# Kernel optimization log

Hardware: AMD Instinct MI355X
Metric: run time of the kernel (lower is better)

Reference implementation:

```python
import jax, jax.numpy as jnp
import numpy as np

STRIDE = (1, 1)
PADDING = (1, 1)
DILATION = (1, 1)


def deform_conv(x, offset, weight, stride=STRIDE, padding=PADDING, dilation=DILATION):
    """Deformable convolution v1 (mmcv layout), deformable_groups=1, groups=1.

    x:      [B, C, H, W]
    offset: [B, 2*kh*kw, Ho, Wo]   pairs ordered (dy, dx) per kernel tap
    weight: [Co, C, kh, kw]
    """
    B, C, H, W = x.shape
    Co, Ci, kh, kw = weight.shape
    sh, sw = stride
    ph, pw = padding
    dh, dw = dilation
    Ho = (H + 2 * ph - (dh * (kh - 1) + 1)) // sh + 1
    Wo = (W + 2 * pw - (dw * (kw - 1) + 1)) // sw + 1
    K2 = kh * kw

    off = offset.reshape(B, K2, 2, Ho, Wo)
    # base sampling grid per kernel tap: [K2, Ho, Wo]
    ky = (jnp.arange(K2) // kw) * dh          # kernel row offsets
    kx = (jnp.arange(K2) % kw) * dw           # kernel col offsets
    hi = jnp.arange(Ho) * sh - ph             # output-row -> input-row base
    wi = jnp.arange(Wo) * sw - pw
    py = off[:, :, 0] + (ky[:, None, None] + hi[None, :, None])  # [B,K2,Ho,Wo]
    px = off[:, :, 1] + (kx[:, None, None] + wi[None, None, :])  # [B,K2,Ho,Wo]

    y0 = jnp.floor(py)
    x0 = jnp.floor(px)
    ly = py - y0
    lx = px - x0
    hy = 1.0 - ly
    hx = 1.0 - lx
    y0i = y0.astype(jnp.int32)
    x0i = x0.astype(jnp.int32)
    y1i = y0i + 1
    x1i = x0i + 1

    xf = x.reshape(B, C, H * W)

    def gather(yi, xi):
        # zero padding outside the image, per-corner validity (DCN semantics)
        valid = (yi >= 0) & (yi < H) & (xi >= 0) & (xi < W)
        yc = jnp.clip(yi, 0, H - 1)
        xc = jnp.clip(xi, 0, W - 1)
        idx = (yc * W + xc).reshape(B, -1)                 # [B, K2*Ho*Wo]
        vals = jax.vmap(lambda xb, ib: xb[:, ib])(xf, idx)  # [B, C, K2*Ho*Wo]
        vals = vals.reshape(B, C, K2, Ho, Wo)
        return vals * valid[:, None].astype(x.dtype)

    # im2col with bilinear sampling: [B, C, K2, Ho, Wo]
    col = (gather(y0i, x0i) * (hy * hx)[:, None]
           + gather(y0i, x1i) * (hy * lx)[:, None]
           + gather(y1i, x0i) * (ly * hx)[:, None]
           + gather(y1i, x1i) * (ly * lx)[:, None])

    # GEMM: out[b,o,h,w] = sum_{c,k} W[o,c,k] * col[b,c,k,h,w]
    out = jnp.einsum('bckhw,ock->bohw', col, weight.reshape(Co, Ci, K2))
    return out


def setup_inputs() -> dict:
    key = jax.random.key(0)
    k1, k2, k3 = jax.random.split(key, 3)
    x = jax.random.normal(k1, (4, 256, 64, 64), dtype=jnp.float32)
    offset = jax.random.normal(k2, (4, 18, 64, 64), dtype=jnp.float32)
    n = 256 * 3 * 3
    stdv = 1.0 / np.sqrt(n)
    weight = jax.random.uniform(k3, (256, 256, 3, 3), dtype=jnp.float32,
                                minval=-stdv, maxval=stdv)
    return {"x": x, "offset": offset, "weight": weight}


def reference(x, offset, weight):
    return deform_conv(x, offset, weight)
```

## Files before the change

### kernel.cpp

```cpp
#include <hip/hip_runtime.h>
#include <hip/hip_bf16.h>
#include <cstddef>

#define B_    4
#define C_    256
#define H_    64
#define W_    64
#define CO_   256
#define K2_   9
#define NSTEP 72

typedef __attribute__((ext_vector_type(8))) short short8;
typedef __attribute__((ext_vector_type(4))) float f32x4;

__device__ __forceinline__ unsigned short f2bf(float f) {
    unsigned u = __builtin_bit_cast(unsigned, f);
    u = (u + 0x7fffu + ((u >> 16) & 1u)) >> 16;
    return (unsigned short)u;
}
__device__ __forceinline__ unsigned pack2bf(float lo, float hi) {
    __hip_bfloat162 h = __float22bfloat162_rn(make_float2(lo, hi));
    unsigned r; __builtin_memcpy(&r, &h, 4);
    return r;
}
__device__ __forceinline__ float bflo(unsigned u) {
    return __builtin_bit_cast(float, u << 16);
}
__device__ __forceinline__ float bfhi(unsigned u) {
    return __builtin_bit_cast(float, u & 0xffff0000u);
}

#if defined(__has_builtin)
#if __has_builtin(__builtin_amdgcn_fdot2_f32_bf16)
#define HAS_BFDOT2 1
#endif
#endif
__device__ __forceinline__ float dot2bf(unsigned x, unsigned w, float acc) {
#ifdef HAS_BFDOT2
    typedef __attribute__((ext_vector_type(2))) __bf16 bf16x2;
    return __builtin_amdgcn_fdot2_f32_bf16(__builtin_bit_cast(bf16x2, x),
                                           __builtin_bit_cast(bf16x2, w),
                                           acc, false);
#else
    return acc + bflo(x) * bflo(w) + bfhi(x) * bfhi(w);
#endif
}

__global__ void wpack_kernel(const float* __restrict__ w,
                             unsigned short* __restrict__ wpk) {
    const int idx = blockIdx.x * 256 + threadIdx.x;
    if (idx >= NSTEP * 16 * 64) return;
    const int lane = idx & 63;
    const int mt   = (idx >> 6) & 15;
    const int s    = idx >> 10;
    const int o    = mt * 16 + (lane & 15);
    const int cc   = s / 9;
    const int t    = s - 9 * cc;
    const int c0   = cc * 32 + ((lane >> 4) << 3);
    unsigned short h[8];
#pragma unroll
    for (int e = 0; e < 8; ++e)
        h[e] = f2bf(w[(o * C_ + c0 + e) * K2_ + t]);
    uint4 v;
    v.x = h[0] | ((unsigned)h[1] << 16);
    v.y = h[2] | ((unsigned)h[3] << 16);
    v.z = h[4] | ((unsigned)h[5] << 16);
    v.w = h[6] | ((unsigned)h[7] << 16);
    *reinterpret_cast<uint4*>(&wpk[(size_t)idx * 8]) = v;
}

__device__ __forceinline__ short8 loadA(const unsigned short* __restrict__ wpk,
                                        const float* __restrict__ wraw,
                                        int use_pk, int s, int mt, int lane) {
    if (use_pk) {
        return *reinterpret_cast<const short8*>(
            wpk + (((size_t)(s * 16 + mt) * 64 + lane) << 3));
    } else {
        const int cc = s / 9;
        const int t  = s - 9 * cc;
        const int c0 = cc * 32 + ((lane >> 4) << 3);
        const int o  = mt * 16 + (lane & 15);
        short8 r;
#pragma unroll
        for (int e = 0; e < 8; ++e)
            r[e] = (short)f2bf(wraw[(o * C_ + c0 + e) * K2_ + t]);
        return r;
    }
}

__global__ __launch_bounds__(512, 4)
void dcn_mfma_kernel(const float* __restrict__ x,
                     const float* __restrict__ off,
                     const unsigned short* __restrict__ wpk,
                     const float* __restrict__ wraw,
                     float* __restrict__ out,
                     int use_pk) {
    __shared__ __align__(16) unsigned s_win[32 * 484 + 48];
    __shared__ __align__(8)  unsigned s_mwp[K2_ * 32 * 2];
    __shared__ int s_menc[K2_ * 32];
    __shared__ __align__(16) unsigned short s_colb[2][1024];

    const int tid = threadIdx.x;
    const int bid = blockIdx.x;
    const int xcd  = bid & 7;
    const int slot = bid >> 3;
    const int b    = xcd >> 1;
    const int ho   = ((xcd & 1) << 5) | (slot >> 1);
    const int woh  = slot & 1;
    const int wo0  = woh << 5;

    const char* xb8 = (const char*)x + ((size_t)b << 22);

    if (tid < 48) s_win[32 * 484 + tid] = 0u;

    if (tid < K2_ * 32) {
        const int t = tid >> 5;
        const int p = tid & 31;
        const int pa = wo0 + p;
        const float dy = off[((b * 18 + 2 * t    ) * 64 + ho) * 64 + pa];
        const float dx = off[((b * 18 + 2 * t + 1) * 64 + ho) * 64 + pa];
        const float py = (float)(ho - 1 + t / 3) + dy;
        const float px = (float)(pa - 1 + t % 3) + dx;
        const float y0f = floorf(py), x0f = floorf(px);
        const float ly = py - y0f, lx = px - x0f;
        const float hy = 1.0f - ly, hx = 1.0f - lx;
        const int y0 = (int)y0f, x0 = (int)x0f;
        const int y1 = y0 + 1,   x1 = x0 + 1;
        const bool vy0 = (y0 >= 0) & (y0 < H_);
        const bool vy1 = (y1 >= 0) & (y1 < H_);
        const bool vx0 = (x0 >= 0) & (x0 < W_);
        const bool vx1 = (x1 >= 0) & (x1 < W_);
        const int yc0 = min(max(y0, 0), H_ - 1);
        const int yc1 = min(max(y1, 0), H_ - 1);
        const int xc0 = min(max(x0, 0), W_ - 1);
        const int xc1 = min(max(x1, 0), W_ - 1);
        float w00 = (vy0 && vx0) ? hy * hx : 0.0f;
        float w01 = (vy0 && vx1) ? hy * lx : 0.0f;
        float w10 = (vy1 && vx0) ? ly * hx : 0.0f;
        float w11 = (vy1 && vx1) ? ly * lx : 0.0f;
        const int dys = yc1 - yc0, dxs = xc1 - xc0;
        if (!dxs) { w00 += w01; w01 = 0.0f; w10 += w11; w11 = 0.0f; }
        if (!dys) { w00 += w10; w10 = 0.0f; w01 += w11; w11 = 0.0f; }
        const int r0 = yc0 - (ho - 5);
        const int j0 = xc0 - (wo0 - 8);
        const bool fast = (r0 >= 0) & (r0 + dys <= 10) & (j0 >= 0) & (j0 <= 43);
        int enc;
        if (fast)
            enc = (r0 * 44 + j0) << 2;
        else
            enc = (int)(0x80000000u
                        | (unsigned)((((yc0 << 6) + xc0) << 2) | (dys << 1) | dxs));
        s_mwp[(t * 32 + p) * 2    ] = pack2bf(w00, w01);
        s_mwp[(t * 32 + p) * 2 + 1] = pack2bf(w10, w11);
        s_menc[t * 32 + p] = enc;
    }

    unsigned stoff[8];
#pragma unroll
    for (int v = 0; v < 8; ++v) {
        const int u = tid + (v << 9);
        if (u < 3872) {
            const int cl  = u / 121;
            const int rem = u - cl * 121;
            const int r   = rem / 11;
            const int q   = rem - r * 11;
            const int y   = ho - 5 + r;
            int gof = (((y << 6) + wo0 - 8) << 2) + (q << 4);
            gof = min(max(gof, 0), 16368);
            if ((unsigned)y >= 64u) gof = 0;
            stoff[v] = ((unsigned)cl << 14) + (unsigned)gof;
        } else {
            stoff[v] = 0xffffffffu;
        }
    }

    const int lane = tid & 63;
    const int wave = tid >> 6;
    const int wo   = lane & 31;
    const int kk0  = (wave << 2) | ((lane >> 5) << 1);
    const unsigned swr = ((unsigned)(wo >> 4) << 10)
                       | ((unsigned)((wo & 15) | ((kk0 >> 3) << 4)) << 4)
                       | ((unsigned)(kk0 & 7) << 1);
    const unsigned brd = (unsigned)lane << 4;
    const int mt0 = wave << 1;
    const char* winC = (const char*)s_win + kk0 * 1936;
    const char* winD = winC + 1936;

    f32x4 acc[2][2];
#pragma unroll
    for (int m = 0; m < 2; ++m)
#pragma unroll
        for (int nt = 0; nt < 2; ++nt)
            acc[m][nt] = (f32x4)(0.0f);

#define STAGEW(XCB_) do {                                                      \
        char* wb_ = (char*)s_win + (size_t)tid * 16;                           \
        _Pragma("unroll")                                                      \
        for (int v_ = 0; v_ < 8; ++v_) {                                       \
            const unsigned so_ = stoff[v_];                                    \
            if (so_ != 0xffffffffu) {                                          \
                const float4 g_ = *(const float4*)((XCB_) + so_);              \
                const unsigned in_ = so_ & 16383u;                             \
                const float g4_ = *(const float*)((XCB_)                       \
                                    + (in_ >= 16368u ? so_ : so_ + 16));       \
                uint4 pk_;                                                     \
                pk_.x = pack2bf(g_.x, g_.y);                                   \
                pk_.y = pack2bf(g_.y, g_.z);                                   \
                pk_.z = pack2bf(g_.z, g_.w);                                   \
                pk_.w = pack2bf(g_.w, g4_);                                    \
                *(uint4*)(wb_ + v_ * 8192) = pk_;                              \
            }                                                                  \
        }                                                                      \
    } while (0)

#define COLT1(T_, BUFB_, XCB_) do {                                            \
        const unsigned u01_ = s_mwp[((T_) * 32 + wo) * 2];                     \
        const unsigned u23_ = s_mwp[((T_) * 32 + wo) * 2 + 1];                 \
        const int mb_ = s_menc[(T_) * 32 + wo];                                \
        float vA_, vB_;                                                        \
        if (__builtin_expect(mb_ >= 0, 1)) {                                   \
            const char* pA_ = winC + mb_;                                      \
            const char* pB_ = winD + mb_;                                      \
            const unsigned a0_ = *(const unsigned*)(pA_);                      \
            const unsigned a1_ = *(const unsigned*)(pA_ + 176);                \
            const unsigned c0_ = *(const unsigned*)(pB_);                      \
            const unsigned c1_ = *(const unsigned*)(pB_ + 176);                \
            vA_ = dot2bf(a1_, u23_, dot2bf(a0_, u01_, 0.0f));                  \
            vB_ = dot2bf(c1_, u23_, dot2bf(c0_, u01_, 0.0f));                  \
        } else {                                                               \
            const float w0_ = bflo(u01_), w1_ = bfhi(u01_);                    \
            const float w2_ = bflo(u23_), w3_ = bfhi(u23_);                    \
            const int dxb_ = (mb_ & 1) << 2, dyb_ = (mb_ & 2) << 7;            \
            const int o_ = mb_ & 0x3fffc;                                      \
            const char* plA_ = (XCB_) + ((size_t)kk0 << 14);                   \
            const char* plB_ = plA_ + (1 << 14);                               \
            vA_ = w0_ * *(const float*)(plA_ + o_)                             \
                + w1_ * *(const float*)(plA_ + o_ + dxb_)                      \
                + w2_ * *(const float*)(plA_ + o_ + dyb_)                      \
                + w3_ * *(const float*)(plA_ + o_ + dyb_ + dxb_);              \
            vB_ = w0_ * *(const float*)(plB_ + o_)                             \
                + w1_ * *(const float*)(plB_ + o_ + dxb_)                      \
                + w2_ * *(const float*)(plB_ + o_ + dyb_)                      \
                + w3_ * *(const float*)(plB_ + o_ + dyb_ + dxb_);              \
        }                                                                      \
        *(unsigned*)((char*)(BUFB_) + swr) = pack2bf(vA_, vB_);                \
    } while (0)

#define MFMA_(A_, B_, C_) __builtin_amdgcn_mfma_f32_16x16x32_bf16(A_, B_, C_, 0, 0, 0)

#define GEMM22(BUFB_) do {                                                     \
        const char* cb_ = (const char*)(BUFB_);                                \
        const short8 b0_ = *(const short8*)(cb_ + brd);                        \
        const short8 b1_ = *(const short8*)(cb_ + brd + 1024);                 \
        acc[0][0] = MFMA_(aC0, b0_, acc[0][0]);                                \
        acc[0][1] = MFMA_(aC0, b1_, acc[0][1]);                                \
        acc[1][0] = MFMA_(aC1, b0_, acc[1][0]);                                \
        acc[1][1] = MFMA_(aC1, b1_, acc[1][1]);                                \
    } while (0)

#define BARLG() do {                                                           \
        asm volatile("s_waitcnt lgkmcnt(0)" ::: "memory");                     \
        __builtin_amdgcn_s_barrier();                                          \
    } while (0)

    char* const buf0 = (char*)s_colb;
    char* const buf1 = (char*)s_colb + 2048;

    STAGEW(xb8);
    __syncthreads();
    COLT1(0, buf0, xb8);
    short8 aC0 = loadA(wpk, wraw, use_pk, 0, mt0,     lane);
    short8 aC1 = loadA(wpk, wraw, use_pk, 0, mt0 + 1, lane);
    BARLG();

    for (int cc = 0; cc < 8; ++cc) {
        const char* xcb  = xb8 + ((size_t)cc << 19);
        const char* xcbN = xb8 + ((size_t)(cc + 1) << 19);

#pragma unroll
        for (int j = 0; j < 9; ++j) {
            const int sj = cc * 9 + j;
            short8 aN0, aN1;
            const bool pf = (sj + 1 < NSTEP);
            if (pf) {
                aN0 = loadA(wpk, wraw, use_pk, sj + 1, mt0,     lane);
                aN1 = loadA(wpk, wraw, use_pk, sj + 1, mt0 + 1, lane);
            }
            if (j < 8) COLT1(j + 1, (j & 1) ? buf0 : buf1, xcb);
            GEMM22((j & 1) ? buf1 : buf0);
            BARLG();
            if (pf) { aC0 = aN0; aC1 = aN1; }
        }

        if (cc < 7) {
            STAGEW(xcbN);
            __syncthreads();
            COLT1(0, buf0, xcbN);
            BARLG();
        }
    }

#undef STAGEW
#undef COLT1
#undef MFMA_
#undef GEMM22
#undef BARLG

#pragma unroll
    for (int m = 0; m < 2; ++m) {
        const int ob = (mt0 + m) * 16 + ((lane >> 4) << 2);
#pragma unroll
        for (int r = 0; r < 4; ++r) {
            float* orow = out + (((size_t)(b * CO_ + ob + r) * 64 + ho) * 64 + wo0);
#pragma unroll
            for (int nt = 0; nt < 2; ++nt)
                orow[(nt << 4) | (lane & 15)] = acc[m][nt][r];
        }
    }
}

extern "C" void kernel_launch(void* const* d_in, const int* in_sizes, int n_in,
                              void* d_out, int out_size, void* d_ws, size_t ws_size,
                              hipStream_t stream) {
    const float* x      = (const float*)d_in[0];
    const float* offset = (const float*)d_in[1];
    const float* weight = (const float*)d_in[2];
    float* out = (float*)d_out;

    const size_t pk_bytes = (size_t)NSTEP * 16 * 64 * 8 * 2;
    const int use_pk = (ws_size >= pk_bytes) ? 1 : 0;
    unsigned short* wpk = (unsigned short*)d_ws;

    if (use_pk) {
        wpack_kernel<<<288, 256, 0, stream>>>(weight, wpk);
    }
    dcn_mfma_kernel<<<512, 512, 0, stream>>>(x, offset, wpk, weight, out, use_pk);
}
```

Measured before the change: 67.22 us.

## Process three kernel taps per barrier phase and overlap window staging with GEMM

Changes the per-tap double-buffered pipeline into phases of three taps, using triple-slot col buffers in each of two banks. This cuts the barrier count per channel chunk from about 9 to 4. The next chunk's window staging (STAGEW) now runs alongside the last phase's MFMAs instead of in a separate serialized step, which also removes one __syncthreads. In exchange the LDS col buffer grows threefold and more A-fragment registers are live at once, which could lower occupancy under launch_bounds(512,4).

```diff
diff --git a/kernel.cpp b/kernel.cpp
--- a/kernel.cpp
+++ b/kernel.cpp
@@ -98,7 +98,7 @@
     __shared__ __align__(16) unsigned s_win[32 * 484 + 48];
     __shared__ __align__(8)  unsigned s_mwp[K2_ * 32 * 2];
     __shared__ int s_menc[K2_ * 32];
-    __shared__ __align__(16) unsigned short s_colb[2][1024];
+    __shared__ __align__(16) unsigned short s_colb[2][3][1024];
 
     const int tid = threadIdx.x;
     const int bid = blockIdx.x;
@@ -213,7 +213,7 @@
         }                                                                      \
     } while (0)
 
-#define COLT1(T_, BUFB_, XCB_) do {                                            \
+#define COLT1(T_, DST_, XCB_) do {                                             \
         const unsigned u01_ = s_mwp[((T_) * 32 + wo) * 2];                     \
         const unsigned u23_ = s_mwp[((T_) * 32 + wo) * 2 + 1];                 \
         const int mb_ = s_menc[(T_) * 32 + wo];                                \
@@ -243,19 +243,19 @@
                 + w2_ * *(const float*)(plB_ + o_ + dyb_)                      \
                 + w3_ * *(const float*)(plB_ + o_ + dyb_ + dxb_);              \
         }                                                                      \
-        *(unsigned*)((char*)(BUFB_) + swr) = pack2bf(vA_, vB_);                \
+        *(unsigned*)((char*)(DST_) + swr) = pack2bf(vA_, vB_);                 \
     } while (0)
 
 #define MFMA_(A_, B_, C_) __builtin_amdgcn_mfma_f32_16x16x32_bf16(A_, B_, C_, 0, 0, 0)
 
-#define GEMM22(BUFB_) do {                                                     \
-        const char* cb_ = (const char*)(BUFB_);                                \
+#define GEMM22(SLOT_, A0_, A1_) do {                                           \
+        const char* cb_ = (const char*)(SLOT_);                                \
         const short8 b0_ = *(const short8*)(cb_ + brd);                        \
         const short8 b1_ = *(const short8*)(cb_ + brd + 1024);                 \
-        acc[0][0] = MFMA_(aC0, b0_, acc[0][0]);                                \
-        acc[0][1] = MFMA_(aC0, b1_, acc[0][1]);                                \
-        acc[1][0] = MFMA_(aC1, b0_, acc[1][0]);                                \
-        acc[1][1] = MFMA_(aC1, b1_, acc[1][1]);                                \
+        acc[0][0] = MFMA_(A0_, b0_, acc[0][0]);                                \
+        acc[0][1] = MFMA_(A0_, b1_, acc[0][1]);                                \
+        acc[1][0] = MFMA_(A1_, b0_, acc[1][0]);                                \
+        acc[1][1] = MFMA_(A1_, b1_, acc[1][1]);                                \
     } while (0)
 
 #define BARLG() do {                                                           \
@@ -263,39 +263,58 @@
         __builtin_amdgcn_s_barrier();                                          \
     } while (0)
 
-    char* const buf0 = (char*)s_colb;
-    char* const buf1 = (char*)s_colb + 2048;
+#define PHASE3(TC_, CDST_, TG_, GSRC_, XCB_) do {                              \
+        const short8 a00_ = loadA(wpk, wraw, use_pk, s0 + (TG_),     mt0,     lane); \
+        const short8 a01_ = loadA(wpk, wraw, use_pk, s0 + (TG_),     mt0 + 1, lane); \
+        const short8 a10_ = loadA(wpk, wraw, use_pk, s0 + (TG_) + 1, mt0,     lane); \
+        const short8 a11_ = loadA(wpk, wraw, use_pk, s0 + (TG_) + 1, mt0 + 1, lane); \
+        const short8 a20_ = loadA(wpk, wraw, use_pk, s0 + (TG_) + 2, mt0,     lane); \
+        const short8 a21_ = loadA(wpk, wraw, use_pk, s0 + (TG_) + 2, mt0 + 1, lane); \
+        COLT1((TC_),     (char*)(CDST_),        XCB_);                         \
+        COLT1((TC_) + 1, (char*)(CDST_) + 2048, XCB_);                         \
+        COLT1((TC_) + 2, (char*)(CDST_) + 4096, XCB_);                         \
+        GEMM22((char*)(GSRC_),        a00_, a01_);                             \
+        GEMM22((char*)(GSRC_) + 2048, a10_, a11_);                             \
+        GEMM22((char*)(GSRC_) + 4096, a20_, a21_);                             \
+        BARLG();                                                               \
+    } while (0)
 
     STAGEW(xb8);
     __syncthreads();
-    COLT1(0, buf0, xb8);
-    short8 aC0 = loadA(wpk, wraw, use_pk, 0, mt0,     lane);
-    short8 aC1 = loadA(wpk, wraw, use_pk, 0, mt0 + 1, lane);
+    COLT1(0, (char*)s_colb,        xb8);
+    COLT1(1, (char*)s_colb + 2048, xb8);
+    COLT1(2, (char*)s_colb + 4096, xb8);
     BARLG();
 
     for (int cc = 0; cc < 8; ++cc) {
         const char* xcb  = xb8 + ((size_t)cc << 19);
         const char* xcbN = xb8 + ((size_t)(cc + 1) << 19);
-
-#pragma unroll
-        for (int j = 0; j < 9; ++j) {
-            const int sj = cc * 9 + j;
-            short8 aN0, aN1;
-            const bool pf = (sj + 1 < NSTEP);
-            if (pf) {
-                aN0 = loadA(wpk, wraw, use_pk, sj + 1, mt0,     lane);
-                aN1 = loadA(wpk, wraw, use_pk, sj + 1, mt0 + 1, lane);
-            }
-            if (j < 8) COLT1(j + 1, (j & 1) ? buf0 : buf1, xcb);
-            GEMM22((j & 1) ? buf1 : buf0);
+        char* bufP = (char*)s_colb + (cc & 1) * 6144;
+        char* bufQ = (char*)s_colb + ((cc & 1) ^ 1) * 6144;
+        const int s0 = cc * 9;
+
+        PHASE3(3, bufQ, 0, bufP, xcb);
+
+        PHASE3(6, bufP, 3, bufQ, xcb);
+
+        {
+            const short8 a00_ = loadA(wpk, wraw, use_pk, s0 + 6, mt0,     lane);
+            const short8 a01_ = loadA(wpk, wraw, use_pk, s0 + 6, mt0 + 1, lane);
+            const short8 a10_ = loadA(wpk, wraw, use_pk, s0 + 7, mt0,     lane);
+            const short8 a11_ = loadA(wpk, wraw, use_pk, s0 + 7, mt0 + 1, lane);
+            const short8 a20_ = loadA(wpk, wraw, use_pk, s0 + 8, mt0,     lane);
+            const short8 a21_ = loadA(wpk, wraw, use_pk, s0 + 8, mt0 + 1, lane);
+            if (cc < 7) STAGEW(xcbN);
+            GEMM22(bufP,        a00_, a01_);
+            GEMM22(bufP + 2048, a10_, a11_);
+            GEMM22(bufP + 4096, a20_, a21_);
             BARLG();
-            if (pf) { aC0 = aN0; aC1 = aN1; }
         }
 
         if (cc < 7) {
-            STAGEW(xcbN);
-            __syncthreads();
-            COLT1(0, buf0, xcbN);
+            COLT1(0, bufQ,        xcbN);
+            COLT1(1, bufQ + 2048, xcbN);
+            COLT1(2, bufQ + 4096, xcbN);
             BARLG();
         }
     }
@@ -305,6 +324,7 @@
 #undef MFMA_
 #undef GEMM22
 #undef BARLG
+#undef PHASE3
 
 #pragma unroll
     for (int m = 0; m < 2; ++m) {
```

New measurement: 65.74 us. 1.02x faster.

## Batch all nine column taps per channel chunk and shrink staging window

Applied to the files above, without the earlier changes.

Each channel chunk now has all nine bilinear column tiles computed into nine LDS buffers at once. The GEMM then runs nine MFMA steps back-to-back with one barrier, replacing nine barriers per chunk. The next chunk's input window is staged into LDS while the GEMM reads the column buffers. The window drops from 11 to 10 rows, trimming LDS footprint and staging loads; more taps' samples may now take the slow global path. Weight-fragment prefetch is removed and fragments are loaded inline in the GEMM loop, which may expose load latency.

```diff
diff --git a/kernel.cpp b/kernel.cpp
--- a/kernel.cpp
+++ b/kernel.cpp
@@ -95,10 +95,10 @@
                      const float* __restrict__ wraw,
                      float* __restrict__ out,
                      int use_pk) {
-    __shared__ __align__(16) unsigned s_win[32 * 484 + 48];
+    __shared__ __align__(16) unsigned s_win[32 * 440 + 48];
     __shared__ __align__(8)  unsigned s_mwp[K2_ * 32 * 2];
     __shared__ int s_menc[K2_ * 32];
-    __shared__ __align__(16) unsigned short s_colb[2][1024];
+    __shared__ __align__(16) unsigned short s_colb[9][1024];
 
     const int tid = threadIdx.x;
     const int bid = blockIdx.x;
@@ -111,7 +111,7 @@
 
     const char* xb8 = (const char*)x + ((size_t)b << 22);
 
-    if (tid < 48) s_win[32 * 484 + tid] = 0u;
+    if (tid < 48) s_win[32 * 440 + tid] = 0u;
 
     if (tid < K2_ * 32) {
         const int t = tid >> 5;
@@ -141,9 +141,9 @@
         const int dys = yc1 - yc0, dxs = xc1 - xc0;
         if (!dxs) { w00 += w01; w01 = 0.0f; w10 += w11; w11 = 0.0f; }
         if (!dys) { w00 += w10; w10 = 0.0f; w01 += w11; w11 = 0.0f; }
-        const int r0 = yc0 - (ho - 5);
+        const int r0 = yc0 - (ho - 4);
         const int j0 = xc0 - (wo0 - 8);
-        const bool fast = (r0 >= 0) & (r0 + dys <= 10) & (j0 >= 0) & (j0 <= 43);
+        const bool fast = (r0 >= 0) & (r0 + dys <= 9) & (j0 >= 0) & (j0 <= 43);
         int enc;
         if (fast)
             enc = (r0 * 44 + j0) << 2;
@@ -155,16 +155,16 @@
         s_menc[t * 32 + p] = enc;
     }
 
-    unsigned stoff[8];
-#pragma unroll
-    for (int v = 0; v < 8; ++v) {
+    unsigned stoff[7];
+#pragma unroll
+    for (int v = 0; v < 7; ++v) {
         const int u = tid + (v << 9);
-        if (u < 3872) {
-            const int cl  = u / 121;
-            const int rem = u - cl * 121;
+        if (u < 3520) {
+            const int cl  = u / 110;
+            const int rem = u - cl * 110;
             const int r   = rem / 11;
             const int q   = rem - r * 11;
-            const int y   = ho - 5 + r;
+            const int y   = ho - 4 + r;
             int gof = (((y << 6) + wo0 - 8) << 2) + (q << 4);
             gof = min(max(gof, 0), 16368);
             if ((unsigned)y >= 64u) gof = 0;
@@ -183,8 +183,8 @@
                        | ((unsigned)(kk0 & 7) << 1);
     const unsigned brd = (unsigned)lane << 4;
     const int mt0 = wave << 1;
-    const char* winC = (const char*)s_win + kk0 * 1936;
-    const char* winD = winC + 1936;
+    const char* winC = (const char*)s_win + kk0 * 1760;
+    const char* winD = winC + 1760;
 
     f32x4 acc[2][2];
 #pragma unroll
@@ -196,7 +196,7 @@
 #define STAGEW(XCB_) do {                                                      \
         char* wb_ = (char*)s_win + (size_t)tid * 16;                           \
         _Pragma("unroll")                                                      \
-        for (int v_ = 0; v_ < 8; ++v_) {                                       \
+        for (int v_ = 0; v_ < 7; ++v_) {                                       \
             const unsigned so_ = stoff[v_];                                    \
             if (so_ != 0xffffffffu) {                                          \
                 const float4 g_ = *(const float4*)((XCB_) + so_);              \
@@ -213,7 +213,7 @@
         }                                                                      \
     } while (0)
 
-#define COLT1(T_, BUFB_, XCB_) do {                                            \
+#define COLT1(T_, XCB_) do {                                                   \
         const unsigned u01_ = s_mwp[((T_) * 32 + wo) * 2];                     \
         const unsigned u23_ = s_mwp[((T_) * 32 + wo) * 2 + 1];                 \
         const int mb_ = s_menc[(T_) * 32 + wo];                                \
@@ -243,67 +243,59 @@
                 + w2_ * *(const float*)(plB_ + o_ + dyb_)                      \
                 + w3_ * *(const float*)(plB_ + o_ + dyb_ + dxb_);              \
         }                                                                      \
-        *(unsigned*)((char*)(BUFB_) + swr) = pack2bf(vA_, vB_);                \
+        *(unsigned*)((char*)s_colb + (T_) * 2048 + swr) = pack2bf(vA_, vB_);   \
     } while (0)
 
 #define MFMA_(A_, B_, C_) __builtin_amdgcn_mfma_f32_16x16x32_bf16(A_, B_, C_, 0, 0, 0)
-
-#define GEMM22(BUFB_) do {                                                     \
-        const char* cb_ = (const char*)(BUFB_);                                \
-        const short8 b0_ = *(const short8*)(cb_ + brd);                        \
-        const short8 b1_ = *(const short8*)(cb_ + brd + 1024);                 \
-        acc[0][0] = MFMA_(aC0, b0_, acc[0][0]);                                \
-        acc[0][1] = MFMA_(aC0, b1_, acc[0][1]);                                \
-        acc[1][0] = MFMA_(aC1, b0_, acc[1][0]);                                \
-        acc[1][1] = MFMA_(aC1, b1_, acc[1][1]);                                \
-    } while (0)
 
 #define BARLG() do {                                                           \
         asm volatile("s_waitcnt lgkmcnt(0)" ::: "memory");                     \
         __builtin_amdgcn_s_barrier();                                          \
     } while (0)
 
-    char* const buf0 = (char*)s_colb;
-    char* const buf1 = (char*)s_colb + 2048;
+#define GEMM9(S0_) do {                                                        \
+        _Pragma("unroll")                                                      \
+        for (int j_ = 0; j_ < 9; ++j_) {                                       \
+            const short8 a0_ = loadA(wpk, wraw, use_pk, (S0_) + j_, mt0,     lane); \
+            const short8 a1_ = loadA(wpk, wraw, use_pk, (S0_) + j_, mt0 + 1, lane); \
+            const char* cb_ = (const char*)s_colb + j_ * 2048;                 \
+            const short8 b0_ = *(const short8*)(cb_ + brd);                    \
+            const short8 b1_ = *(const short8*)(cb_ + brd + 1024);             \
+            acc[0][0] = MFMA_(a0_, b0_, acc[0][0]);                            \
+            acc[0][1] = MFMA_(a0_, b1_, acc[0][1]);                            \
+            acc[1][0] = MFMA_(a1_, b0_, acc[1][0]);                            \
+            acc[1][1] = MFMA_(a1_, b1_, acc[1][1]);                            \
+        }                                                                      \
+    } while (0)
+
+#define COLT9(XCB_) do {                                                       \
+        _Pragma("unroll")                                                      \
+        for (int t_ = 0; t_ < 9; ++t_) COLT1(t_, XCB_);                        \
+    } while (0)
 
     STAGEW(xb8);
     __syncthreads();
-    COLT1(0, buf0, xb8);
-    short8 aC0 = loadA(wpk, wraw, use_pk, 0, mt0,     lane);
-    short8 aC1 = loadA(wpk, wraw, use_pk, 0, mt0 + 1, lane);
+    COLT9(xb8);
     BARLG();
 
     for (int cc = 0; cc < 8; ++cc) {
-        const char* xcb  = xb8 + ((size_t)cc << 19);
         const char* xcbN = xb8 + ((size_t)(cc + 1) << 19);
 
-#pragma unroll
-        for (int j = 0; j < 9; ++j) {
-            const int sj = cc * 9 + j;
-            short8 aN0, aN1;
-            const bool pf = (sj + 1 < NSTEP);
-            if (pf) {
-                aN0 = loadA(wpk, wraw, use_pk, sj + 1, mt0,     lane);
-                aN1 = loadA(wpk, wraw, use_pk, sj + 1, mt0 + 1, lane);
-            }
-            if (j < 8) COLT1(j + 1, (j & 1) ? buf0 : buf1, xcb);
-            GEMM22((j & 1) ? buf1 : buf0);
-            BARLG();
-            if (pf) { aC0 = aN0; aC1 = aN1; }
-        }
+        if (cc < 7) STAGEW(xcbN);
+        GEMM9(cc * 9);
+        BARLG();
 
         if (cc < 7) {
-            STAGEW(xcbN);
-            __syncthreads();
-            COLT1(0, buf0, xcbN);
+            COLT9(xcbN);
             BARLG();
         }
     }
 
 #undef STAGEW
 #undef COLT1
+#undef COLT9
 #undef MFMA_
-#undef GEMM22
+#undef GEMM9
 #undef BARLG
 
 #pragma unroll
```

Result: no change. 67.77 us (+0.8%).
